# Optimization experiments

Measured on AMD Instinct MI355X. Metric: run time of the kernel, lower is better.

The kernel has to match this reference:

```python
import jax, jax.numpy as jnp
import numpy as np


def setup_inputs() -> dict:
    key = jax.random.key(0)
    k1, k2, k3 = jax.random.split(key, 3)
    B, C, P, T = 8, 256, 16, 64
    H = 8
    d = C // H  # 32
    x = jax.random.normal(k1, (B, C, P, T), dtype=jnp.float32)
    # per-head 1x1 conv weights: project C -> d channels (Q=K=V share this conv)
    W = jax.random.normal(k2, (H, d, C), dtype=jnp.float32) * (1.0 / np.sqrt(C))
    b = jax.random.normal(k3, (H, d), dtype=jnp.float32) * 0.01
    return {"x": x, "W": W, "b": b}


def reference(x, W, b):
    B, C, P, T = x.shape
    H, d, _ = W.shape
    L = P * T
    # per-head 1x1 conv == channel contraction; Q = K = V = z
    z = jnp.einsum('bcpt,hdc->bhptd', x, W) + b[None, :, None, None, :]
    z = z.reshape(B, H, L, d)
    scale = 1.0 / jnp.sqrt(jnp.asarray(d, dtype=z.dtype))
    scores = jax.nn.softmax(jnp.einsum('bhld,bhmd->bhlm', z, z) * scale, axis=-1)
    out = jnp.einsum('bhlm,bhmd->bhld', scores, z)  # (B,H,L,d)
    # reshape back to (B, P, T, d) per head, permute to channels-first, cat heads
    out = out.reshape(B, H, P, T, d).transpose(0, 1, 4, 2, 3).reshape(B, H * d, P, T)
    return out
```

## Files before the change

kernel.cpp:

```cpp
#include <hip/hip_runtime.h>
#include <math.h>

#define BB 8
#define CC 256
#define LL 1024
#define HH 8
#define DD 32

typedef __attribute__((ext_vector_type(8))) short bf16x8;
typedef __attribute__((ext_vector_type(16))) float f32x16;

#if __has_builtin(__builtin_amdgcn_exp2f)
#define EXP2F(x) __builtin_amdgcn_exp2f(x)
#else
#define EXP2F(x) exp2f(x)
#endif

__device__ inline unsigned pk2bf(float a, float b) {
  unsigned ua = __float_as_uint(a), ub = __float_as_uint(b);
  ua += 0x7FFFu + ((ua >> 16) & 1u);
  ub += 0x7FFFu + ((ub >> 16) & 1u);
  return (ua >> 16) | (ub & 0xFFFF0000u);
}

__device__ inline unsigned pk2bf_fast(float a, float b) {
  unsigned ua = __float_as_uint(a) + 0x8000u;
  unsigned ub = __float_as_uint(b) + 0x8000u;
  return __builtin_amdgcn_perm(ub, ua, 0x07060302u);
}

__global__ __launch_bounds__(256) void w16_kernel(
    const float* __restrict__ W, unsigned short* __restrict__ w16f) {
  int f = blockIdx.x * 256 + threadIdx.x;
  int lane = f & 63;
  int ks = (f >> 6) & 15;
  int head = f >> 10;
  int n = lane & 31, h = lane >> 5;
  const float* src = W + (size_t)(head * 32 + n) * CC + ks * 16 + h * 8;
  float4 a = *(const float4*)src;
  float4 c = *(const float4*)(src + 4);
  uint4 v;
  v.x = pk2bf(a.x, a.y);
  v.y = pk2bf(a.z, a.w);
  v.z = pk2bf(c.x, c.y);
  v.w = pk2bf(c.z, c.w);
  ((uint4*)w16f)[f] = v;
}

__global__ __launch_bounds__(256) void proj_mfma(
    const float* __restrict__ x, const unsigned short* __restrict__ w16f,
    const float* __restrict__ bias, unsigned short* __restrict__ z16,
    unsigned short* __restrict__ zT16) {
  __shared__ unsigned short smem[64 * 264];

  int b = blockIdx.x >> 6;
  int rem = blockIdx.x & 63;
  int lc = rem >> 2;
  int hg = rem & 3;
  int l0 = lc * 64;
  int tid = threadIdx.x;
  int lane = tid & 63;
  int w = tid >> 6;

  {
    const float* xb = x + (size_t)b * CC * LL + (l0 + lane);
    unsigned short* row = &smem[lane * 264];
#pragma unroll 8
    for (int i = 0; i < 32; ++i) {
      int c0 = w * 64 + 2 * i;
      float f0 = xb[(size_t)c0 * LL];
      float f1 = xb[(size_t)(c0 + 1) * LL];
      *(unsigned*)&row[c0] = pk2bf_fast(f0, f1);
    }
  }
  __syncthreads();

  int n = lane & 31, h = lane >> 5;
  int lt = w & 1;
  int lh = w >> 1;
  int head = hg * 2 + lh;

  f32x16 acc = 0.0f;
  const unsigned short* xrow = &smem[(lt * 32 + n) * 264];
  const unsigned short* wf = w16f + ((size_t)head * 16) * 64 * 8;
#pragma unroll
  for (int ks = 0; ks < 16; ++ks) {
    bf16x8 bfrag = *(const bf16x8*)(xrow + ks * 16 + h * 8);
    bf16x8 afrag = *(const bf16x8*)(wf + ((size_t)ks * 64 + lane) * 8);
    acc = __builtin_amdgcn_mfma_f32_32x32x16_bf16(afrag, bfrag, acc, 0, 0, 0);
  }

  unsigned pkk[8];
  const float* bp = bias + head * DD;
#pragma unroll
  for (int g = 0; g < 4; ++g) {
    int ddb = 8 * g + 4 * h;
    float f0 = acc[4 * g + 0] + bp[ddb + 0];
    float f1 = acc[4 * g + 1] + bp[ddb + 1];
    float f2 = acc[4 * g + 2] + bp[ddb + 2];
    float f3 = acc[4 * g + 3] + bp[ddb + 3];
    unsigned p0 = pk2bf_fast(f0, f1);
    unsigned p1 = pk2bf_fast(f2, f3);
    pkk[2 * g] = p0;
    pkk[2 * g + 1] = p1;
    size_t base = (((size_t)b * HH + head) * DD + ddb) * LL + l0 + lt * 32 + n;
    zT16[base + 0 * LL] = (unsigned short)(p0 & 0xFFFFu);
    zT16[base + 1 * LL] = (unsigned short)(p0 >> 16);
    zT16[base + 2 * LL] = (unsigned short)(p1 & 0xFFFFu);
    zT16[base + 3 * LL] = (unsigned short)(p1 >> 16);
  }

  __syncthreads();
#pragma unroll
  for (int g = 0; g < 4; ++g) {
    unsigned short* zr = &smem[(lt * 32 + n) * 72 + lh * 32 + 8 * g + 4 * h];
    *(unsigned*)&zr[0] = pkk[2 * g];
    *(unsigned*)&zr[2] = pkk[2 * g + 1];
  }
  __syncthreads();

  {
    int l = tid >> 2, q = tid & 3;
    const unsigned short* src = &smem[l * 72 + q * 16];
    uint4 v0 = *(const uint4*)src;
    uint4 v1 = *(const uint4*)(src + 8);
    int headl = hg * 2 + (q >> 1);
    int dd0 = (q & 1) * 16;
    unsigned short* dst =
        z16 + (((size_t)b * HH + headl) * LL + l0 + l) * DD + dd0;
    *(uint4*)dst = v0;
    *(uint4*)(dst + 8) = v1;
  }
}

__global__ __launch_bounds__(256, 4) void attn_mfma(
    const unsigned short* __restrict__ z, const unsigned short* __restrict__ zT,
    float* __restrict__ out) {
  __shared__ float mrg[2][64][17];

  int lane = threadIdx.x & 63;
  int wave = threadIdx.x >> 6;
  int qg = wave & 1;
  int ksp = wave >> 1;
  int m = lane & 31;
  int h = lane >> 5;
  int bh = blockIdx.x >> 4;
  int qbase = (blockIdx.x & 15) * 64 + qg * 32;

  const unsigned short* zb = z + (size_t)bh * LL * DD;
  const unsigned short* zTb = zT + (size_t)bh * DD * LL;

  bf16x8 qf0 = *(const bf16x8*)(zb + (size_t)(qbase + m) * DD + h * 8);
  bf16x8 qf1 = *(const bf16x8*)(zb + (size_t)(qbase + m) * DD + 16 + h * 8);

  f32x16 O = 0.0f;
  float sum0 = 0.0f, sum1 = 0.0f;
  const float Cn2 = 0.25506441211245744f;

  int kstart = ksp * 512;
#pragma unroll 2
  for (int t = 0; t < 16; ++t) {
    int kb = kstart + t * 32;
    bf16x8 kf0 = *(const bf16x8*)(zb + (size_t)(kb + m) * DD + h * 8);
    bf16x8 kf1 = *(const bf16x8*)(zb + (size_t)(kb + m) * DD + 16 + h * 8);
    bf16x8 vf0 = *(const bf16x8*)(zTb + (size_t)m * LL + kb + h * 8);
    bf16x8 vf1 = *(const bf16x8*)(zTb + (size_t)m * LL + kb + 16 + h * 8);

    f32x16 sv = 0.0f;
    sv = __builtin_amdgcn_mfma_f32_32x32x16_bf16(kf0, qf0, sv, 0, 0, 0);
    sv = __builtin_amdgcn_mfma_f32_32x32x16_bf16(kf1, qf1, sv, 0, 0, 0);

    float ps[16];
#pragma unroll
    for (int r = 0; r < 16; ++r) ps[r] = EXP2F(sv[r] * Cn2);
#pragma unroll
    for (int r = 0; r < 16; r += 2) {
      sum0 += ps[r];
      sum1 += ps[r + 1];
    }

    unsigned pk[8];
#pragma unroll
    for (int g = 0; g < 4; ++g) {
      pk[2 * g] = pk2bf_fast(ps[4 * g], ps[4 * g + 1]);
      pk[2 * g + 1] = pk2bf_fast(ps[4 * g + 2], ps[4 * g + 3]);
    }
#pragma unroll
    for (int h2 = 0; h2 < 2; ++h2) {
      unsigned s0 = h ? pk[4 * h2] : pk[4 * h2 + 2];
      unsigned s1 = h ? pk[4 * h2 + 1] : pk[4 * h2 + 3];
      unsigned r0 = __shfl_xor(s0, 32, 64);
      unsigned r1 = __shfl_xor(s1, 32, 64);
      unsigned e0 = h ? r0 : pk[4 * h2];
      unsigned e1 = h ? r1 : pk[4 * h2 + 1];
      unsigned e2 = h ? pk[4 * h2 + 2] : r0;
      unsigned e3 = h ? pk[4 * h2 + 3] : r1;
      union { unsigned u[4]; bf16x8 v; } pf;
      pf.u[0] = e0; pf.u[1] = e1; pf.u[2] = e2; pf.u[3] = e3;
      O = __builtin_amdgcn_mfma_f32_32x32x16_bf16(h2 ? vf1 : vf0, pf.v, O, 0,
                                                  0, 0);
    }
  }

  float ssum = sum0 + sum1;

  if (ksp) {
#pragma unroll
    for (int r = 0; r < 16; ++r) mrg[qg][lane][r] = O[r];
    mrg[qg][lane][16] = ssum;
  }
  __syncthreads();
  if (!ksp) {
#pragma unroll
    for (int r = 0; r < 16; ++r) O[r] += mrg[qg][lane][r];
    ssum += mrg[qg][lane][16];
    ssum += __shfl_xor(ssum, 32, 64);
    float inv = 1.0f / ssum;
#pragma unroll
    for (int r = 0; r < 16; ++r) {
      int dd = (r & 3) + 8 * (r >> 2) + 4 * h;
      out[((size_t)bh * DD + dd) * LL + qbase + m] = O[r] * inv;
    }
  }
}

extern "C" void kernel_launch(void* const* d_in, const int* in_sizes, int n_in,
                              void* d_out, int out_size, void* d_ws,
                              size_t ws_size, hipStream_t stream) {
  const float* x = (const float*)d_in[0];
  const float* W = (const float*)d_in[1];
  const float* bias = (const float*)d_in[2];
  float* out = (float*)d_out;

  unsigned short* z16 = (unsigned short*)d_ws;
  unsigned short* zT16 = z16 + (size_t)BB * HH * LL * DD;
  unsigned short* w16f = zT16 + (size_t)BB * HH * LL * DD;

  hipLaunchKernelGGL(w16_kernel, dim3(32), dim3(256), 0, stream, W, w16f);
  hipLaunchKernelGGL(proj_mfma, dim3(512), dim3(256), 0, stream, x, w16f,
                     bias, z16, zT16);
  hipLaunchKernelGGL(attn_mfma, dim3(BB * HH * (LL / 64)), dim3(256), 0,
                     stream, z16, zT16, out);
}
```

Measured before the change: 96.64 us.

## Fold softmax scale into Q and restructure projection to load x once per block

The projection kernel now uses 512-thread blocks that compute all 8 heads for 32 positions. Each x tile is therefore read and converted once instead of being reloaded by four head-group blocks, at the cost of half as many blocks. In attention, the softmax scale is pre-multiplied into the bf16 Q fragments, removing a multiply per score element, which adds one extra bf16 rounding on Q. The row-sum accumulation is also written as a packed float2 add so the compiler can emit packed FP32 math.

```diff
diff --git a/kernel.cpp b/kernel.cpp
--- a/kernel.cpp
+++ b/kernel.cpp
@@ -8,6 +8,7 @@
 #define DD 32
 
 typedef __attribute__((ext_vector_type(8))) short bf16x8;
+typedef __attribute__((ext_vector_type(2))) float f32x2;
 typedef __attribute__((ext_vector_type(16))) float f32x16;
 
 #if __has_builtin(__builtin_amdgcn_exp2f)
@@ -47,41 +48,35 @@
   ((uint4*)w16f)[f] = v;
 }
 
-__global__ __launch_bounds__(256) void proj_mfma(
+__global__ __launch_bounds__(512) void proj_mfma(
     const float* __restrict__ x, const unsigned short* __restrict__ w16f,
     const float* __restrict__ bias, unsigned short* __restrict__ z16,
     unsigned short* __restrict__ zT16) {
-  __shared__ unsigned short smem[64 * 264];
-
-  int b = blockIdx.x >> 6;
-  int rem = blockIdx.x & 63;
-  int lc = rem >> 2;
-  int hg = rem & 3;
-  int l0 = lc * 64;
+  __shared__ unsigned short smem[32 * 264];
+
+  int b = blockIdx.x >> 5;
+  int l0 = (blockIdx.x & 31) * 32;
   int tid = threadIdx.x;
+
+  {
+    int l = tid & 31, cg = tid >> 5;
+    const float* xb = x + (size_t)b * CC * LL + l0 + l;
+    unsigned short* row = &smem[l * 264 + cg * 16];
+#pragma unroll
+    for (int i = 0; i < 16; i += 2) {
+      float f0 = xb[(size_t)(cg * 16 + i) * LL];
+      float f1 = xb[(size_t)(cg * 16 + i + 1) * LL];
+      *(unsigned*)&row[i] = pk2bf_fast(f0, f1);
+    }
+  }
+  __syncthreads();
+
   int lane = tid & 63;
-  int w = tid >> 6;
-
-  {
-    const float* xb = x + (size_t)b * CC * LL + (l0 + lane);
-    unsigned short* row = &smem[lane * 264];
-#pragma unroll 8
-    for (int i = 0; i < 32; ++i) {
-      int c0 = w * 64 + 2 * i;
-      float f0 = xb[(size_t)c0 * LL];
-      float f1 = xb[(size_t)(c0 + 1) * LL];
-      *(unsigned*)&row[c0] = pk2bf_fast(f0, f1);
-    }
-  }
-  __syncthreads();
-
+  int head = tid >> 6;
   int n = lane & 31, h = lane >> 5;
-  int lt = w & 1;
-  int lh = w >> 1;
-  int head = hg * 2 + lh;
 
   f32x16 acc = 0.0f;
-  const unsigned short* xrow = &smem[(lt * 32 + n) * 264];
+  const unsigned short* xrow = &smem[n * 264];
   const unsigned short* wf = w16f + ((size_t)head * 16) * 64 * 8;
 #pragma unroll
   for (int ks = 0; ks < 16; ++ks) {
@@ -103,7 +98,7 @@
     unsigned p1 = pk2bf_fast(f2, f3);
     pkk[2 * g] = p0;
     pkk[2 * g + 1] = p1;
-    size_t base = (((size_t)b * HH + head) * DD + ddb) * LL + l0 + lt * 32 + n;
+    size_t base = (((size_t)b * HH + head) * DD + ddb) * LL + l0 + n;
     zT16[base + 0 * LL] = (unsigned short)(p0 & 0xFFFFu);
     zT16[base + 1 * LL] = (unsigned short)(p0 >> 16);
     zT16[base + 2 * LL] = (unsigned short)(p1 & 0xFFFFu);
@@ -113,21 +108,20 @@
   __syncthreads();
 #pragma unroll
   for (int g = 0; g < 4; ++g) {
-    unsigned short* zr = &smem[(lt * 32 + n) * 72 + lh * 32 + 8 * g + 4 * h];
+    unsigned short* zr = &smem[n * 264 + head * 32 + 8 * g + 4 * h];
     *(unsigned*)&zr[0] = pkk[2 * g];
     *(unsigned*)&zr[2] = pkk[2 * g + 1];
   }
   __syncthreads();
 
   {
-    int l = tid >> 2, q = tid & 3;
-    const unsigned short* src = &smem[l * 72 + q * 16];
+    int hh = tid >> 6, r = tid & 63;
+    int l = r >> 1, half = r & 1;
+    const unsigned short* src = &smem[l * 264 + hh * 32 + half * 16];
     uint4 v0 = *(const uint4*)src;
     uint4 v1 = *(const uint4*)(src + 8);
-    int headl = hg * 2 + (q >> 1);
-    int dd0 = (q & 1) * 16;
     unsigned short* dst =
-        z16 + (((size_t)b * HH + headl) * LL + l0 + l) * DD + dd0;
+        z16 + (((size_t)b * HH + hh) * LL + l0 + l) * DD + half * 16;
     *(uint4*)dst = v0;
     *(uint4*)(dst + 8) = v1;
   }
@@ -150,12 +144,28 @@
   const unsigned short* zb = z + (size_t)bh * LL * DD;
   const unsigned short* zTb = zT + (size_t)bh * DD * LL;
 
-  bf16x8 qf0 = *(const bf16x8*)(zb + (size_t)(qbase + m) * DD + h * 8);
-  bf16x8 qf1 = *(const bf16x8*)(zb + (size_t)(qbase + m) * DD + 16 + h * 8);
+  const float Cn2 = 0.25506441211245744f;
+
+  bf16x8 qf0, qf1;
+  {
+    union { unsigned u[4]; bf16x8 v; } a, c;
+    a.v = *(const bf16x8*)(zb + (size_t)(qbase + m) * DD + h * 8);
+    c.v = *(const bf16x8*)(zb + (size_t)(qbase + m) * DD + 16 + h * 8);
+#pragma unroll
+    for (int j = 0; j < 4; ++j) {
+      float lo = __uint_as_float(a.u[j] << 16) * Cn2;
+      float hi = __uint_as_float(a.u[j] & 0xFFFF0000u) * Cn2;
+      a.u[j] = pk2bf(lo, hi);
+      float lo2 = __uint_as_float(c.u[j] << 16) * Cn2;
+      float hi2 = __uint_as_float(c.u[j] & 0xFFFF0000u) * Cn2;
+      c.u[j] = pk2bf(lo2, hi2);
+    }
+    qf0 = a.v;
+    qf1 = c.v;
+  }
 
   f32x16 O = 0.0f;
-  float sum0 = 0.0f, sum1 = 0.0f;
-  const float Cn2 = 0.25506441211245744f;
+  f32x2 sum2 = {0.0f, 0.0f};
 
   int kstart = ksp * 512;
 #pragma unroll 2
@@ -170,20 +180,19 @@
     sv = __builtin_amdgcn_mfma_f32_32x32x16_bf16(kf0, qf0, sv, 0, 0, 0);
     sv = __builtin_amdgcn_mfma_f32_32x32x16_bf16(kf1, qf1, sv, 0, 0, 0);
 
-    float ps[16];
-#pragma unroll
-    for (int r = 0; r < 16; ++r) ps[r] = EXP2F(sv[r] * Cn2);
+#pragma unroll
+    for (int r = 0; r < 16; ++r) sv[r] = EXP2F(sv[r]);
 #pragma unroll
     for (int r = 0; r < 16; r += 2) {
-      sum0 += ps[r];
-      sum1 += ps[r + 1];
+      f32x2 pr = {sv[r], sv[r + 1]};
+      sum2 += pr;
     }
 
     unsigned pk[8];
 #pragma unroll
     for (int g = 0; g < 4; ++g) {
-      pk[2 * g] = pk2bf_fast(ps[4 * g], ps[4 * g + 1]);
-      pk[2 * g + 1] = pk2bf_fast(ps[4 * g + 2], ps[4 * g + 3]);
+      pk[2 * g] = pk2bf_fast(sv[4 * g], sv[4 * g + 1]);
+      pk[2 * g + 1] = pk2bf_fast(sv[4 * g + 2], sv[4 * g + 3]);
     }
 #pragma unroll
     for (int h2 = 0; h2 < 2; ++h2) {
@@ -202,7 +211,7 @@
     }
   }
 
-  float ssum = sum0 + sum1;
+  float ssum = sum2.x + sum2.y;
 
   if (ksp) {
 #pragma unroll
@@ -237,7 +246,7 @@
   unsigned short* w16f = zT16 + (size_t)BB * HH * LL * DD;
 
   hipLaunchKernelGGL(w16_kernel, dim3(32), dim3(256), 0, stream, W, w16f);
-  hipLaunchKernelGGL(proj_mfma, dim3(512), dim3(256), 0, stream, x, w16f,
+  hipLaunchKernelGGL(proj_mfma, dim3(BB * 32), dim3(512), 0, stream, x, w16f,
                      bias, z16, zT16);
   hipLaunchKernelGGL(attn_mfma, dim3(BB * HH * (LL / 64)), dim3(256), 0,
                      stream, z16, zT16, out);
```

Result: faster. 94.48 us (-2.2%).
